# Optimization experiments

Hardware: AMD Instinct MI355X
Metric: run time of the kernel (lower is better)

The kernel has to match this reference:

```python
import jax, jax.numpy as jnp
import numpy as np


def setup_inputs() -> dict:
    key = jax.random.key(0)
    ks = jax.random.split(key, 7)
    B, N, Fin, Fout = 32, 1024, 64, 64
    s = 1.0 / np.sqrt(Fin)
    return {
        "X": jax.random.normal(ks[0], (B, N, Fin), dtype=jnp.float32),
        "A": jax.random.normal(ks[1], (B, N, N), dtype=jnp.float32),  # unused in forward, kept for signature fidelity
        "W": jax.random.uniform(ks[2], (Fin, Fout), jnp.float32, -s, s),
        "att_W": jax.random.uniform(ks[3], (Fin, Fout), jnp.float32, -s, s),
        "a": jax.random.uniform(ks[4], (Fout, Fout), jnp.float32, -s, s),
        "bias_W": jax.random.uniform(ks[5], (Fout,), jnp.float32, -s, s),
        "self_W": jax.random.uniform(ks[6], (Fin, Fout), jnp.float32, -s, s),
    }


def reference(X, A, W, att_W, a, bias_W, self_W):
    # att_X = X @ att_W : [B, N, Fout]
    att_X = jnp.einsum('bnf,fg->bng', X, att_W)
    # torch einsum 'ij,ajk->ajk' sums `a` over i => per-feature scale a.sum(0)
    scale = jnp.sum(a, axis=0)  # [Fout]
    # Z[b,i,k] = sum_j att_X[b,i,j] * scale[j] * att_X[b,k,j]  -> [B, N, N]
    Z = jnp.einsum('big,bkg->bik', att_X * scale, att_X)
    n = Z.shape[1]
    Z = Z * (1.0 - jnp.eye(n, dtype=Z.dtype))  # zero diagonal per batch
    att = jax.nn.leaky_relu(Z, negative_slope=0.01)
    # H = att @ (X W) + bias_W + X self_W
    XW = jnp.einsum('bnf,fg->bng', X, W)
    H = jnp.einsum('bnm,bmg->bng', att, XW) + bias_W
    H = H + jnp.einsum('bnf,fg->bng', X, self_W)
    return H
```

## Files before the change

### kernel.cpp

```cpp
#include <hip/hip_runtime.h>

#define DEV __device__ __forceinline__
typedef short s16x8 __attribute__((ext_vector_type(8)));
typedef float f32x16 __attribute__((ext_vector_type(16)));
typedef unsigned short u16;

#define WAIT_VMCNT(N) asm volatile("s_waitcnt vmcnt(" #N ")" ::: "memory")
#define CFENCE asm volatile("" ::: "memory")

DEV unsigned cvt_pk_bf16(float lo, float hi) {
  unsigned r;
  asm volatile("v_cvt_pk_bf16_f32 %0, %1, %2" : "=v"(r) : "v"(lo), "v"(hi));
  return r;
}
DEV u16 f2bf(float f) {
  unsigned u = __builtin_bit_cast(unsigned, f);
  unsigned r = u + 0x7fffu + ((u >> 16) & 1u);
  return (u16)(r >> 16);
}
DEV float bf2f(u16 u) { return __builtin_bit_cast(float, (unsigned)u << 16); }
DEV f32x16 zero16() {
  f32x16 v;
  #pragma unroll
  for (int i = 0; i < 16; ++i) v[i] = 0.f;
  return v;
}

DEV void gld16(const u16* g, u16* l) {
  __builtin_amdgcn_global_load_lds(
      (const __attribute__((address_space(1))) void*)g,
      (__attribute__((address_space(3))) void*)l, 16, 0, 0);
}

DEV void stage_tile64(const u16* __restrict__ gbase, size_t stride, u16* lbuf, int t) {
  #pragma unroll
  for (int p = 0; p < 2; ++p) {
    int c = p * 256 + t;
    int row = c >> 3, s = c & 7;
    int gck = s ^ (row & 7);
    const u16* src = gbase + (size_t)row * stride + gck * 8;
    u16* dst = lbuf + (size_t)(p * 256 + (t & 192)) * 8;
    gld16(src, dst);
  }
}

DEV s16x8 frag(const u16* buf, int row, int chunk) {
  return *(const s16x8*)(buf + row * 64 + ((chunk ^ (row & 7)) << 3));
}

DEV int kswz(int row, int d) {
  return row * 64 + ((((d >> 3) ^ (row & 7)) << 3) | (d & 7));
}

DEV void stage_wt(const float* __restrict__ src, u16* dst, int t) {
  #pragma unroll
  for (int r = 0; r < 4; ++r) {
    int e = (r * 256 + t) * 4;
    int f = e >> 6, g0 = e & 63;
    float4 v = *(const float4*)(src + f * 64 + g0);
    float vv[4] = {v.x, v.y, v.z, v.w};
    #pragma unroll
    for (int j = 0; j < 4; ++j) {
      int g = g0 + j;
      dst[g * 64 + ((((f >> 3) ^ (g & 7)) << 3) | (f & 7))] = f2bf(vv[j]);
    }
  }
}

__global__ __launch_bounds__(256) void prep_kernel(
    const float* __restrict__ X, const float* __restrict__ W,
    const float* __restrict__ attW, const float* __restrict__ Aa,
    const float* __restrict__ biasW, const float* __restrict__ selfW,
    u16* __restrict__ Kbf, u16* __restrict__ Vt, u16* __restrict__ Bb,
    float* __restrict__ scal_ws) {
  __shared__ __align__(16) u16 Xl[64 * 64];
  __shared__ __align__(16) u16 Wt[3][64 * 64];
  __shared__ __align__(16) u16 Bl[64 * 64];
  __shared__ __align__(16) u16 Vl[64 * 72];
  __shared__ float sc4[4][64];

  const int t = threadIdx.x;
  const int b = blockIdx.x;
  const int n0 = blockIdx.y * 64;
  const int r0 = b * 1024 + n0;
  const bool sblk = (blockIdx.x == 0 && blockIdx.y == 0);
  const int lane = t & 63, w = t >> 6, h = lane >> 5, ln = lane & 31;
  const int rg = (w >> 1) * 32;
  const int cf = w & 1;
  const int d = cf * 32 + ln;

  if (sblk) {
    int qt = t >> 6, dd = t & 63;
    float s = 0.f;
    #pragma unroll
    for (int i = 0; i < 16; ++i) s += Aa[(qt * 16 + i) * 64 + dd];
    sc4[qt][dd] = s;
  }

  #pragma unroll
  for (int p = 0; p < 2; ++p) {
    int c = p * 256 + t;
    int row = c >> 3, ck = c & 7;
    const float4* src = (const float4*)(X + (size_t)(r0 + row) * 64 + ck * 8);
    float4 a0 = src[0], a1 = src[1];
    unsigned* dst = (unsigned*)&Xl[row * 64 + ((ck ^ (row & 7)) << 3)];
    dst[0] = cvt_pk_bf16(a0.x, a0.y);
    dst[1] = cvt_pk_bf16(a0.z, a0.w);
    dst[2] = cvt_pk_bf16(a1.x, a1.y);
    dst[3] = cvt_pk_bf16(a1.z, a1.w);
  }
  stage_wt(attW, &Wt[0][0], t);
  stage_wt(W, &Wt[1][0], t);
  stage_wt(selfW, &Wt[2][0], t);
  __syncthreads();

  s16x8 xa[4];
  #pragma unroll
  for (int ks = 0; ks < 4; ++ks) xa[ks] = frag(Xl, rg + ln, ks * 2 + h);

  f32x16 aA = zero16(), aW = zero16(), aS = zero16();
  #pragma unroll
  for (int ks = 0; ks < 4; ++ks) {
    s16x8 bA = frag(&Wt[0][0], d, ks * 2 + h);
    s16x8 bW = frag(&Wt[1][0], d, ks * 2 + h);
    s16x8 bS = frag(&Wt[2][0], d, ks * 2 + h);
    aA = __builtin_amdgcn_mfma_f32_32x32x16_bf16(xa[ks], bA, aA, 0, 0, 0);
    aW = __builtin_amdgcn_mfma_f32_32x32x16_bf16(xa[ks], bW, aW, 0, 0, 0);
    aS = __builtin_amdgcn_mfma_f32_32x32x16_bf16(xa[ks], bS, aS, 0, 0, 0);
  }
  __syncthreads();

  const float bi = biasW[d];
  #pragma unroll
  for (int reg = 0; reg < 16; ++reg) {
    int rl = (reg & 3) + 8 * (reg >> 2) + 4 * h;
    int row = rg + rl;
    Xl[kswz(row, d)] = f2bf(aA[reg]);
    Bl[kswz(row, d)] = f2bf(aS[reg] + bi);
  }
  #pragma unroll
  for (int pg = 0; pg < 4; ++pg) {
    int n = rg + pg * 8 + 4 * h;
    *(unsigned*)&Vl[d * 72 + n] = cvt_pk_bf16(aW[pg * 4 + 0], aW[pg * 4 + 1]);
    *(unsigned*)&Vl[d * 72 + n + 2] = cvt_pk_bf16(aW[pg * 4 + 2], aW[pg * 4 + 3]);
  }
  __syncthreads();

  #pragma unroll
  for (int p = 0; p < 2; ++p) {
    int c = p * 256 + t;
    int row = c >> 3, ck = c & 7;
    size_t go = (size_t)(r0 + row) * 64 + ck * 8;
    int lo = row * 64 + ((ck ^ (row & 7)) << 3);
    *(s16x8*)&Kbf[go] = *(const s16x8*)&Xl[lo];
    *(s16x8*)&Bb[go] = *(const s16x8*)&Bl[lo];
  }
  #pragma unroll
  for (int p = 0; p < 2; ++p) {
    int c = p * 256 + t;
    int dd = c >> 3, ck = c & 7;
    *(s16x8*)&Vt[(size_t)(b * 64 + dd) * 1024 + n0 + ck * 8] =
        *(const s16x8*)&Vl[dd * 72 + ck * 8];
  }
  if (sblk && t < 64)
    scal_ws[t] = sc4[0][t] + sc4[1][t] + sc4[2][t] + sc4[3][t];
}

#define PROC(SV, DG, PWV)                                                      \
  do {                                                                         \
    float p_[16];                                                              \
    _Pragma("unroll") for (int r_ = 0; r_ < 16; ++r_) {                        \
      float v_ = (SV)[r_];                                                     \
      p_[r_] = fmaxf(v_, 0.01f * v_);                                          \
    }                                                                          \
    if (DG) {                                                                  \
      _Pragma("unroll") for (int r_ = 0; r_ < 16; ++r_) {                      \
        int rl_ = (r_ & 3) + 8 * (r_ >> 2) + 4 * h;                            \
        p_[r_] = (rl_ == ln) ? 0.f : p_[r_];                                   \
      }                                                                        \
    }                                                                          \
    unsigned pk_[8];                                                           \
    _Pragma("unroll") for (int i_ = 0; i_ < 8; ++i_)                           \
        pk_[i_] = cvt_pk_bf16(p_[2 * i_], p_[2 * i_ + 1]);                     \
    auto a0_ = __builtin_amdgcn_permlane32_swap(pk_[0], pk_[2], false, false); \
    auto a1_ = __builtin_amdgcn_permlane32_swap(pk_[1], pk_[3], false, false); \
    auto a2_ = __builtin_amdgcn_permlane32_swap(pk_[4], pk_[6], false, false); \
    auto a3_ = __builtin_amdgcn_permlane32_swap(pk_[5], pk_[7], false, false); \
    PWV[0][0] = a0_[0]; PWV[0][1] = a1_[0]; PWV[0][2] = a0_[1];                \
    PWV[0][3] = a1_[1]; PWV[1][0] = a2_[0]; PWV[1][1] = a3_[0];                \
    PWV[1][2] = a2_[1]; PWV[1][3] = a3_[1];                                    \
  } while (0)

__global__ __launch_bounds__(256) void attn_kernel(
    const u16* __restrict__ Kbf, const u16* __restrict__ Vt,
    const u16* __restrict__ Bb, const float* __restrict__ scal_ws,
    float* __restrict__ Hout) {
  __shared__ __align__(16) u16 ring[4][2][4096];

  const int t = threadIdx.x;
  const int b = blockIdx.x;
  const int q0 = blockIdx.y * 128;
  const int lane = t & 63, w = t >> 6, h = lane >> 5, ln = lane & 31;
  const int qg = w & 1;
  const int kvh = w >> 1;

  const u16* Kg = Kbf + (size_t)b * 65536;
  const u16* Vg = Vt + (size_t)b * 65536;

  s16x8 qraw[2][4];
  #pragma unroll
  for (int qh = 0; qh < 2; ++qh)
    #pragma unroll
    for (int ks = 0; ks < 4; ++ks)
      qraw[qh][ks] = *(const s16x8*)(
          Kg + (size_t)(q0 + qg * 64 + qh * 32 + ln) * 64 + ks * 16 + h * 8);
  float4 sA[4], sB[4];
  #pragma unroll
  for (int ks = 0; ks < 4; ++ks) {
    sA[ks] = *(const float4*)(scal_ws + ks * 16 + h * 8);
    sB[ks] = *(const float4*)(scal_ws + ks * 16 + h * 8 + 4);
  }

  #pragma unroll
  for (int i = 0; i < 3; ++i) {
    stage_tile64(Kg + (size_t)i * 4096, 64, &ring[i][0][0], t);
    stage_tile64(Vg + i * 64, 1024, &ring[i][1][0], t);
  }

  s16x8 qf[2][4];
  #pragma unroll
  for (int qh = 0; qh < 2; ++qh)
    #pragma unroll
    for (int ks = 0; ks < 4; ++ks) {
      union { unsigned u[4]; s16x8 v; } qq;
      qq.u[0] = cvt_pk_bf16(bf2f((u16)qraw[qh][ks][0]) * sA[ks].x,
                            bf2f((u16)qraw[qh][ks][1]) * sA[ks].y);
      qq.u[1] = cvt_pk_bf16(bf2f((u16)qraw[qh][ks][2]) * sA[ks].z,
                            bf2f((u16)qraw[qh][ks][3]) * sA[ks].w);
      qq.u[2] = cvt_pk_bf16(bf2f((u16)qraw[qh][ks][4]) * sB[ks].x,
                            bf2f((u16)qraw[qh][ks][5]) * sB[ks].y);
      qq.u[3] = cvt_pk_bf16(bf2f((u16)qraw[qh][ks][6]) * sB[ks].z,
                            bf2f((u16)qraw[qh][ks][7]) * sB[ks].w);
      qf[qh][ks] = qq.v;
    }

  WAIT_VMCNT(8);
  __builtin_amdgcn_s_barrier();
  CFENCE;

  s16x8 kf[4];
  #pragma unroll
  for (int ks = 0; ks < 4; ++ks)
    kf[ks] = frag(&ring[0][0][0], kvh * 32 + ln, ks * 2 + h);

  f32x16 o00 = zero16(), o01 = zero16();
  f32x16 o10 = zero16(), o11 = zero16();

  #pragma unroll 1
  for (int i = 0; i < 16; ++i) {
    const int kv0 = i * 64;
    if (i < 14) {
      WAIT_VMCNT(4);
    } else {
      WAIT_VMCNT(0);
    }
    __builtin_amdgcn_s_barrier();
    CFENCE;
    if (i < 13) {
      const int ns = (i + 3) & 3;
      stage_tile64(Kg + (size_t)(i + 3) * 4096, 64, &ring[ns][0][0], t);
      stage_tile64(Vg + (i + 3) * 64, 1024, &ring[ns][1][0], t);
    }
    const u16* Vl = &ring[i & 3][1][0];

    s16x8 vf[2][2];
    #pragma unroll
    for (int dh = 0; dh < 2; ++dh)
      #pragma unroll
      for (int c = 0; c < 2; ++c)
        vf[dh][c] = frag(Vl, dh * 32 + ln, (kvh * 2 + c) * 2 + h);

    f32x16 s0 = zero16(), s1 = zero16();
    __builtin_amdgcn_s_setprio(1);
    #pragma unroll
    for (int ks = 0; ks < 4; ++ks) {
      s0 = __builtin_amdgcn_mfma_f32_32x32x16_bf16(kf[ks], qf[0][ks], s0, 0, 0, 0);
      s1 = __builtin_amdgcn_mfma_f32_32x32x16_bf16(kf[ks], qf[1][ks], s1, 0, 0, 0);
    }
    __builtin_amdgcn_s_setprio(0);

    const bool dg0 = (kv0 + kvh * 32) == (q0 + qg * 64);
    const bool dg1 = (kv0 + kvh * 32) == (q0 + qg * 64 + 32);
    unsigned pw0[2][4], pw1[2][4];
    PROC(s0, dg0, pw0);
    PROC(s1, dg1, pw1);

    if (i < 15) {
      const u16* Kn = &ring[(i + 1) & 3][0][0];
      #pragma unroll
      for (int ks = 0; ks < 4; ++ks)
        kf[ks] = frag(Kn, kvh * 32 + ln, ks * 2 + h);
    }

    __builtin_amdgcn_s_setprio(1);
    #pragma unroll
    for (int c = 0; c < 2; ++c) {
      union { unsigned u[4]; s16x8 v; } pb0, pb1;
      #pragma unroll
      for (int j = 0; j < 4; ++j) { pb0.u[j] = pw0[c][j]; pb1.u[j] = pw1[c][j]; }
      o00 = __builtin_amdgcn_mfma_f32_32x32x16_bf16(vf[0][c], pb0.v, o00, 0, 0, 0);
      o01 = __builtin_amdgcn_mfma_f32_32x32x16_bf16(vf[0][c], pb1.v, o01, 0, 0, 0);
      o10 = __builtin_amdgcn_mfma_f32_32x32x16_bf16(vf[1][c], pb0.v, o10, 0, 0, 0);
      o11 = __builtin_amdgcn_mfma_f32_32x32x16_bf16(vf[1][c], pb1.v, o11, 0, 0, 0);
    }
    __builtin_amdgcn_s_setprio(0);
  }

  __syncthreads();

  float* R0 = (float*)&ring[0][0][0];
  float* R1 = R0 + 4096;
  #pragma unroll
  for (int g = 0; g < 2; ++g) {
    if (qg == g) {
      float* Rd = kvh ? R1 : R0;
      #pragma unroll
      for (int qh = 0; qh < 2; ++qh) {
        const f32x16& oA = qh ? o01 : o00;
        const f32x16& oB = qh ? o11 : o10;
        int q = qh * 32 + ln;
        #pragma unroll
        for (int reg = 0; reg < 16; ++reg) {
          int rl = (reg & 3) + 8 * (reg >> 2) + 4 * h;
          int d0 = rl, d1 = 32 + rl;
          Rd[q * 64 + ((((d0 >> 2) ^ (q & 15)) << 2) | (d0 & 3))] = oA[reg];
          Rd[q * 64 + ((((d1 >> 2) ^ (q & 15)) << 2) | (d1 & 3))] = oB[reg];
        }
      }
    }
    __syncthreads();
    #pragma unroll
    for (int e = 0; e < 4; ++e) {
      int idx = e * 256 + t;
      int q = idx >> 4, dgp = idx & 15;
      int off = q * 64 + ((dgp ^ (q & 15)) << 2);
      float4 v0 = *(const float4*)&R0[off];
      float4 v1 = *(const float4*)&R1[off];
      size_t go = ((size_t)b * 1024 + q0 + g * 64 + q) * 64 + dgp * 4;
      const short4 bv = *(const short4*)(Bb + go);
      float4 v;
      v.x = v0.x + v1.x + bf2f((u16)bv.x);
      v.y = v0.y + v1.y + bf2f((u16)bv.y);
      v.z = v0.z + v1.z + bf2f((u16)bv.z);
      v.w = v0.w + v1.w + bf2f((u16)bv.w);
      *(float4*)(Hout + go) = v;
    }
    if (g == 0) __syncthreads();
  }
}

extern "C" void kernel_launch(void* const* d_in, const int* in_sizes, int n_in,
                              void* d_out, int out_size, void* d_ws, size_t ws_size,
                              hipStream_t stream) {
  const float* X = (const float*)d_in[0];
  const float* W = (const float*)d_in[2];
  const float* attW = (const float*)d_in[3];
  const float* a = (const float*)d_in[4];
  const float* biasW = (const float*)d_in[5];
  const float* selfW = (const float*)d_in[6];
  float* H = (float*)d_out;

  u16* Kbf = (u16*)d_ws;
  u16* Vt = Kbf + (size_t)32 * 1024 * 64;
  u16* Bb = Vt + (size_t)32 * 1024 * 64;
  float* scal = (float*)(Bb + (size_t)32 * 1024 * 64);

  prep_kernel<<<dim3(32, 16), 256, 0, stream>>>(X, W, attW, a, biasW, selfW,
                                                Kbf, Vt, Bb, scal);
  attn_kernel<<<dim3(32, 8), 256, 0, stream>>>(Kbf, Vt, Bb, scal, H);
}
```

Baseline: 33.99 us.

## Write fp32 self+bias term directly into output and accumulate in attention epilogue

The prep kernel now writes the X@selfW+bias term straight into the fp32 output buffer instead of staging it through LDS into a bf16 workspace. The attention epilogue then reads that base from the output and adds to it in place. This removes the bf16 Bb buffer, its LDS staging and a round of rounding, but the scattered per-element fp32 stores and the fp32 read-back double that traffic's byte count. Weight staging is also reworked so each thread packs eight k-values into one 16-byte LDS store rather than doing scalar converted stores.

```diff
diff --git a/kernel.cpp b/kernel.cpp
--- a/kernel.cpp
+++ b/kernel.cpp
@@ -52,18 +52,17 @@
   return row * 64 + ((((d >> 3) ^ (row & 7)) << 3) | (d & 7));
 }
 
-DEV void stage_wt(const float* __restrict__ src, u16* dst, int t) {
-  #pragma unroll
-  for (int r = 0; r < 4; ++r) {
-    int e = (r * 256 + t) * 4;
-    int f = e >> 6, g0 = e & 63;
-    float4 v = *(const float4*)(src + f * 64 + g0);
-    float vv[4] = {v.x, v.y, v.z, v.w};
-    #pragma unroll
-    for (int j = 0; j < 4; ++j) {
-      int g = g0 + j;
-      dst[g * 64 + ((((f >> 3) ^ (g & 7)) << 3) | (f & 7))] = f2bf(vv[j]);
-    }
+DEV void stage_wt2(const float* __restrict__ src, u16* dst, int t) {
+  const int g = t & 63, kk = t >> 6;
+  #pragma unroll
+  for (int p = 0; p < 2; ++p) {
+    const int k8 = kk + p * 4;
+    union { unsigned u[4]; s16x8 v; } pk;
+    #pragma unroll
+    for (int j = 0; j < 4; ++j)
+      pk.u[j] = cvt_pk_bf16(src[(k8 * 8 + 2 * j) * 64 + g],
+                            src[(k8 * 8 + 2 * j + 1) * 64 + g]);
+    *(s16x8*)&dst[g * 64 + ((k8 ^ (g & 7)) << 3)] = pk.v;
   }
 }
 
@@ -71,11 +70,10 @@
     const float* __restrict__ X, const float* __restrict__ W,
     const float* __restrict__ attW, const float* __restrict__ Aa,
     const float* __restrict__ biasW, const float* __restrict__ selfW,
-    u16* __restrict__ Kbf, u16* __restrict__ Vt, u16* __restrict__ Bb,
+    u16* __restrict__ Kbf, u16* __restrict__ Vt, float* __restrict__ Hout,
     float* __restrict__ scal_ws) {
   __shared__ __align__(16) u16 Xl[64 * 64];
   __shared__ __align__(16) u16 Wt[3][64 * 64];
-  __shared__ __align__(16) u16 Bl[64 * 64];
   __shared__ __align__(16) u16 Vl[64 * 72];
   __shared__ float sc4[4][64];
 
@@ -109,9 +107,9 @@
     dst[2] = cvt_pk_bf16(a1.x, a1.y);
     dst[3] = cvt_pk_bf16(a1.z, a1.w);
   }
-  stage_wt(attW, &Wt[0][0], t);
-  stage_wt(W, &Wt[1][0], t);
-  stage_wt(selfW, &Wt[2][0], t);
+  stage_wt2(attW, &Wt[0][0], t);
+  stage_wt2(W, &Wt[1][0], t);
+  stage_wt2(selfW, &Wt[2][0], t);
   __syncthreads();
 
   s16x8 xa[4];
@@ -136,7 +134,7 @@
     int rl = (reg & 3) + 8 * (reg >> 2) + 4 * h;
     int row = rg + rl;
     Xl[kswz(row, d)] = f2bf(aA[reg]);
-    Bl[kswz(row, d)] = f2bf(aS[reg] + bi);
+    Hout[(size_t)(r0 + row) * 64 + d] = aS[reg] + bi;
   }
   #pragma unroll
   for (int pg = 0; pg < 4; ++pg) {
@@ -150,10 +148,8 @@
   for (int p = 0; p < 2; ++p) {
     int c = p * 256 + t;
     int row = c >> 3, ck = c & 7;
-    size_t go = (size_t)(r0 + row) * 64 + ck * 8;
-    int lo = row * 64 + ((ck ^ (row & 7)) << 3);
-    *(s16x8*)&Kbf[go] = *(const s16x8*)&Xl[lo];
-    *(s16x8*)&Bb[go] = *(const s16x8*)&Bl[lo];
+    *(s16x8*)&Kbf[(size_t)(r0 + row) * 64 + ck * 8] =
+        *(const s16x8*)&Xl[row * 64 + ((ck ^ (row & 7)) << 3)];
   }
   #pragma unroll
   for (int p = 0; p < 2; ++p) {
@@ -193,8 +189,7 @@
 
 __global__ __launch_bounds__(256) void attn_kernel(
     const u16* __restrict__ Kbf, const u16* __restrict__ Vt,
-    const u16* __restrict__ Bb, const float* __restrict__ scal_ws,
-    float* __restrict__ Hout) {
+    const float* __restrict__ scal_ws, float* __restrict__ Hout) {
   __shared__ __align__(16) u16 ring[4][2][4096];
 
   const int t = threadIdx.x;
@@ -347,13 +342,14 @@
       float4 v0 = *(const float4*)&R0[off];
       float4 v1 = *(const float4*)&R1[off];
       size_t go = ((size_t)b * 1024 + q0 + g * 64 + q) * 64 + dgp * 4;
-      const short4 bv = *(const short4*)(Bb + go);
+      float4* gp = (float4*)(Hout + go);
+      float4 base = *gp;
       float4 v;
-      v.x = v0.x + v1.x + bf2f((u16)bv.x);
-      v.y = v0.y + v1.y + bf2f((u16)bv.y);
-      v.z = v0.z + v1.z + bf2f((u16)bv.z);
-      v.w = v0.w + v1.w + bf2f((u16)bv.w);
-      *(float4*)(Hout + go) = v;
+      v.x = v0.x + v1.x + base.x;
+      v.y = v0.y + v1.y + base.y;
+      v.z = v0.z + v1.z + base.z;
+      v.w = v0.w + v1.w + base.w;
+      *gp = v;
     }
     if (g == 0) __syncthreads();
   }
@@ -372,10 +368,9 @@
 
   u16* Kbf = (u16*)d_ws;
   u16* Vt = Kbf + (size_t)32 * 1024 * 64;
-  u16* Bb = Vt + (size_t)32 * 1024 * 64;
-  float* scal = (float*)(Bb + (size_t)32 * 1024 * 64);
+  float* scal = (float*)(Vt + (size_t)32 * 1024 * 64);
 
   prep_kernel<<<dim3(32, 16), 256, 0, stream>>>(X, W, attW, a, biasW, selfW,
-                                                Kbf, Vt, Bb, scal);
-  attn_kernel<<<dim3(32, 8), 256, 0, stream>>>(Kbf, Vt, Bb, scal, H);
-}
+                                                Kbf, Vt, H, scal);
+  attn_kernel<<<dim3(32, 8), 256, 0, stream>>>(Kbf, Vt, scal, H);
+}
```

After: 36.47 us. 1.07x slower.
